# Kernel tuning notes

Hardware: AMD Instinct MI355X
Metric: run time of the kernel (lower is better)

Reference implementation:

```python
import jax, jax.numpy as jnp
import numpy as np

H = 64  # hidden_size
IN = 9  # input_size == output_size
PRED_LEN = 10
SRC_LEN = 7
B = 65536


def _lstm_step(x, h, c, Wih, Whh, b):
    # PyTorch gate order: i, f, g, o
    gates = x @ Wih.T + h @ Whh.T + b  # (B, 4H)
    i, f, g, o = jnp.split(gates, 4, axis=-1)
    i = jax.nn.sigmoid(i)
    f = jax.nn.sigmoid(f)
    g = jnp.tanh(g)
    o = jax.nn.sigmoid(o)
    c_new = f * c + i * g
    h_new = o * jnp.tanh(c_new)
    return h_new, c_new


def setup_inputs() -> dict:
    key = jax.random.key(0)
    ks = jax.random.split(key, 9)
    s = 1.0 / np.sqrt(H)  # torch LSTM init scale
    return {
        "src": jax.random.normal(ks[0], (B, SRC_LEN, IN), dtype=jnp.float32),
        "enc_Wih": jax.random.normal(ks[1], (4 * H, IN), dtype=jnp.float32) * s,
        "enc_Whh": jax.random.normal(ks[2], (4 * H, H), dtype=jnp.float32) * s,
        "enc_b": jax.random.normal(ks[3], (4 * H,), dtype=jnp.float32) * s,
        "dec_Wih": jax.random.normal(ks[4], (4 * H, IN), dtype=jnp.float32) * s,
        "dec_Whh": jax.random.normal(ks[5], (4 * H, H), dtype=jnp.float32) * s,
        "dec_b": jax.random.normal(ks[6], (4 * H,), dtype=jnp.float32) * s,
        "fc_W": jax.random.normal(ks[7], (IN, H), dtype=jnp.float32) * s,
        "fc_b": jax.random.normal(ks[8], (IN,), dtype=jnp.float32) * s,
    }


def reference(src, enc_Wih, enc_Whh, enc_b, dec_Wih, dec_Whh, dec_b, fc_W, fc_b):
    b = src.shape[0]
    h0 = jnp.zeros((b, H), dtype=src.dtype)
    c0 = jnp.zeros((b, H), dtype=src.dtype)

    # Encoder: scan over the 7 source timesteps
    def enc_f(carry, x_t):
        h, c = carry
        h, c = _lstm_step(x_t, h, c, enc_Wih, enc_Whh, enc_b)
        return (h, c), None

    (h, c), _ = jax.lax.scan(enc_f, (h0, c0), jnp.swapaxes(src, 0, 1))

    x_last = src[:, -1, :]  # (B, IN)

    def dec_f(carry, _):
        h, c, x = carry
        h, c = _lstm_step(x, h, c, dec_Wih, dec_Whh, dec_b)
        pred = h @ fc_W.T + fc_b  # (B, IN)
        return (h, c, pred), pred

    _, preds = jax.lax.scan(dec_f, (h, c, x_last), None, length=PRED_LEN)
    return jnp.swapaxes(preds, 0, 1)  # (B, PRED_LEN, IN)
```

## Files before the change

kernel.cpp:

```cpp
#include <hip/hip_runtime.h>
#include <hip/hip_bf16.h>
#include <stdint.h>

namespace {
constexpr int kH = 64;
constexpr int kIn = 9;
constexpr int kSrcLen = 7;
constexpr int kPredLen = 10;
constexpr int kRows = 64;
constexpr int kThreads = 256;
constexpr int kOutW = kPredLen * kIn;
constexpr int kABlk = 12;
constexpr int kASz = kABlk * kRows * 8;

typedef __attribute__((ext_vector_type(8))) _Float16 frag_a;
typedef __attribute__((ext_vector_type(4))) float frag_cd;

__device__ __forceinline__ float fast_rcp(float x) { return __builtin_amdgcn_rcpf(x); }
__device__ __forceinline__ float sigmoid_f(float x) { return fast_rcp(1.0f + __expf(-x)); }
__device__ __forceinline__ float tanh_f(float x) { return 1.0f - 2.0f * fast_rcp(__expf(2.0f * x) + 1.0f); }

__device__ __forceinline__ float ldf(const void* p, int i, int isbf) {
  if (isbf) {
    uint32_t w = ((uint32_t)((const uint16_t*)p)[i]) << 16;
    float f; __builtin_memcpy(&f, &w, 4); return f;
  }
  return ((const float*)p)[i];
}

__device__ __forceinline__ float gate_w(const void* Whh, const void* Wih,
                                        int n, int k, int isbf) {
  if (k < kH) return ldf(Whh, n * kH + k, isbf);
  if (k < kH + kIn) return ldf(Wih, n * kIn + (k - kH), isbf);
  return 0.0f;
}
}

extern "C" __global__ void detect_dtype_kernel(const uint16_t* __restrict__ src_u16,
                                               int* __restrict__ flag) {
  const int t = threadIdx.x;
  int bad = 0;
  for (int i = t; i < 256; i += 64) {
    const uint16_t u = src_u16[i];
    const uint32_t e = (u >> 7) & 0xFF;
    const int plausible = (u == 0) || (e >= 100 && e <= 150);
    bad += !plausible;
  }
#pragma unroll
  for (int off = 32; off; off >>= 1) bad += __shfl_down(bad, off, 64);
  if (t == 0) *flag = (bad < 64) ? 1 : 0;
}

extern "C" __global__ void __launch_bounds__(kThreads)
__attribute__((amdgpu_waves_per_eu(2, 2)))
lstm_seq2seq_kernel(const void* __restrict__ src,
                    const void* __restrict__ enc_Wih,
                    const void* __restrict__ enc_Whh,
                    const void* __restrict__ enc_b,
                    const void* __restrict__ dec_Wih,
                    const void* __restrict__ dec_Whh,
                    const void* __restrict__ dec_b,
                    const void* __restrict__ fc_W,
                    const void* __restrict__ fc_b,
                    void* __restrict__ out,
                    const int* __restrict__ flag) {
  __shared__ __align__(16) _Float16 a_m[2][kASz];

  const int tid = threadIdx.x;
  const int lane = tid & 63;
  const int wave = tid >> 6;
  const int quad = lane >> 4;
  const int half = lane & 15;
  const int row0 = blockIdx.x * kRows;
  const int isbf = *flag;
  const int col = wave * 16 + half;

  for (int i = tid; i < kASz; i += kThreads) {
    a_m[0][i] = (_Float16)0.0f;
    a_m[1][i] = (_Float16)0.0f;
  }
  __syncthreads();

  for (int item = tid; item < kRows * kIn; item += kThreads) {
    const int r = item / kIn, i = item - r * kIn;
    const float x = ldf(src, (row0 + r) * (kSrcLen * kIn) + i, isbf);
    a_m[0][(((8 + (i >> 3)) * kRows) + r) * 8 + (i & 7)] = (_Float16)x;
  }

  float c_st[16];
#pragma unroll
  for (int i = 0; i < 16; ++i) c_st[i] = 0.0f;

  frag_a bm[3][4];
  float bias_g[4];
  frag_a fm[2];
  float fcb = 0.0f;

  auto load_gate_frags = [&](const void* Whh, const void* Wih, const void* bv) {
#pragma unroll
    for (int kt = 0; kt < 3; ++kt) {
#pragma unroll
      for (int nt = 0; nt < 4; ++nt) {
        frag_a f;
        const int n = nt * kH + col;
#pragma unroll
        for (int j = 0; j < 8; ++j) {
          const int k = kt * 32 + quad * 8 + j;
          f[j] = (_Float16)gate_w(Whh, Wih, n, k, isbf);
        }
        bm[kt][nt] = f;
      }
    }
#pragma unroll
    for (int nt = 0; nt < 4; ++nt) bias_g[nt] = ldf(bv, nt * kH + col, isbf);
  };

  auto lstm_step = [&](int cur) {
#pragma unroll 1
    for (int ch = 0; ch < 4; ++ch) {
      const int r = ch * 16 + half;
      const frag_a a0 = *(const frag_a*)&a_m[cur][((0 * 4 + quad) * kRows + r) * 8];
      const frag_a a1 = *(const frag_a*)&a_m[cur][((1 * 4 + quad) * kRows + r) * 8];
      const frag_a a2 = *(const frag_a*)&a_m[cur][((2 * 4 + quad) * kRows + r) * 8];

      frag_cd acc[4];
#pragma unroll
      for (int nt = 0; nt < 4; ++nt) {
        const float b = bias_g[nt];
        frag_cd a = {b, b, b, b};
        a = __builtin_amdgcn_mfma_f32_16x16x32_f16(a0, bm[0][nt], a, 0, 0, 0);
        a = __builtin_amdgcn_mfma_f32_16x16x32_f16(a1, bm[1][nt], a, 0, 0, 0);
        a = __builtin_amdgcn_mfma_f32_16x16x32_f16(a2, bm[2][nt], a, 0, 0, 0);
        acc[nt] = a;
      }

#pragma unroll
      for (int j = 0; j < 4; ++j) {
        const float gi = acc[0][j];
        const float gf = acc[1][j];
        const float gg = acc[2][j];
        const float go = acc[3][j];
        float c = c_st[ch * 4 + j];
        c = fmaf(sigmoid_f(gf), c, sigmoid_f(gi) * tanh_f(gg));
        c_st[ch * 4 + j] = c;
        const float h = sigmoid_f(go) * tanh_f(c);
        const int rr = ch * 16 + quad * 4 + j;
        a_m[cur ^ 1][(((col >> 3) * kRows) + rr) * 8 + (col & 7)] = (_Float16)h;
      }
    }
  };

  load_gate_frags(enc_Whh, enc_Wih, enc_b);
  __syncthreads();

  int cur = 0;
#pragma unroll 1
  for (int s = 0; s < kSrcLen; ++s) {
    lstm_step(cur);
    const int ns = (s + 1 < kSrcLen) ? s + 1 : kSrcLen - 1;
    for (int item = tid; item < kRows * kIn; item += kThreads) {
      const int r = item / kIn, i = item - r * kIn;
      const float x = ldf(src, (row0 + r) * (kSrcLen * kIn) + ns * kIn + i, isbf);
      a_m[cur ^ 1][(((8 + (i >> 3)) * kRows) + r) * 8 + (i & 7)] = (_Float16)x;
    }
    __syncthreads();
    cur ^= 1;
  }

  load_gate_frags(dec_Whh, dec_Wih, dec_b);
#pragma unroll
  for (int kt = 0; kt < 2; ++kt) {
    frag_a f;
#pragma unroll
    for (int j = 0; j < 8; ++j) {
      const int k = kt * 32 + quad * 8 + j;
      const float v = (half < kIn) ? ldf(fc_W, half * kH + k, isbf) : 0.0f;
      f[j] = (_Float16)v;
    }
    fm[kt] = f;
  }
  fcb = (half < kIn) ? ldf(fc_b, half, isbf) : 0.0f;

#pragma unroll 1
  for (int t = 0; t < kPredLen; ++t) {
    lstm_step(cur);
    __syncthreads();
    cur ^= 1;

    const int r = wave * 16 + half;
    const frag_a a0 = *(const frag_a*)&a_m[cur][((0 * 4 + quad) * kRows + r) * 8];
    const frag_a a1 = *(const frag_a*)&a_m[cur][((1 * 4 + quad) * kRows + r) * 8];
    frag_cd p = {fcb, fcb, fcb, fcb};
    p = __builtin_amdgcn_mfma_f32_16x16x32_f16(a0, fm[0], p, 0, 0, 0);
    p = __builtin_amdgcn_mfma_f32_16x16x32_f16(a1, fm[1], p, 0, 0, 0);

    if (half < kIn) {
#pragma unroll
      for (int j = 0; j < 4; ++j) {
        const int rr = wave * 16 + quad * 4 + j;
        const float pred = p[j];
        const int oidx = (row0 + rr) * kOutW + t * kIn + half;
        if (isbf) {
          ((__hip_bfloat16*)out)[oidx] = __float2bfloat16(pred);
        } else {
          ((float*)out)[oidx] = pred;
        }
        a_m[cur][(((8 + (half >> 3)) * kRows) + rr) * 8 + (half & 7)] = (_Float16)pred;
      }
    }
    __syncthreads();
  }
}

extern "C" void kernel_launch(void* const* d_in, const int* in_sizes, int n_in,
                              void* d_out, int out_size, void* d_ws, size_t ws_size,
                              hipStream_t stream) {
  (void)n_in; (void)ws_size; (void)out_size;
  int* flag = (int*)d_ws;

  hipLaunchKernelGGL(detect_dtype_kernel, dim3(1), dim3(64), 0, stream,
                     (const uint16_t*)d_in[0], flag);

  const int b_total = in_sizes[0] / (kSrcLen * kIn);
  const int grid = b_total / kRows;

  hipLaunchKernelGGL(lstm_seq2seq_kernel, dim3(grid), dim3(kThreads), 0, stream,
                     d_in[0], d_in[1], d_in[2], d_in[3], d_in[4], d_in[5],
                     d_in[6], d_in[7], d_in[8], d_out, flag);
}
```

Baseline: 255.2 us.

## Fold bias into MFMA via constant-one column, prefetch src loads, raise occupancy

Puts the gate bias into the spare K slot 73 of the weight fragments and sets a constant 1.0 in the matching activation column, so the MFMA accumulators start at zero and no bias registers are needed. The next timestep's src values are now loaded into registers before the LSTM step runs, hiding global-load latency behind the MFMA work. The LDS and global index math is precomputed once per thread. The waves-per-EU hint goes from 2 to 3, which trades registers per thread for occupancy and risks spills given the large fragment arrays.

```diff
diff --git a/kernel.cpp b/kernel.cpp
--- a/kernel.cpp
+++ b/kernel.cpp
@@ -10,6 +10,7 @@
 constexpr int kRows = 64;
 constexpr int kThreads = 256;
 constexpr int kOutW = kPredLen * kIn;
+constexpr int kBiasK = 73;
 constexpr int kABlk = 12;
 constexpr int kASz = kABlk * kRows * 8;
 
@@ -29,9 +30,10 @@
 }
 
 __device__ __forceinline__ float gate_w(const void* Whh, const void* Wih,
-                                        int n, int k, int isbf) {
+                                        const void* bv, int n, int k, int isbf) {
   if (k < kH) return ldf(Whh, n * kH + k, isbf);
   if (k < kH + kIn) return ldf(Wih, n * kIn + (k - kH), isbf);
+  if (k == kBiasK) return ldf(bv, n, isbf);
   return 0.0f;
 }
 }
@@ -52,7 +54,7 @@
 }
 
 extern "C" __global__ void __launch_bounds__(kThreads)
-__attribute__((amdgpu_waves_per_eu(2, 2)))
+__attribute__((amdgpu_waves_per_eu(3, 3)))
 lstm_seq2seq_kernel(const void* __restrict__ src,
                     const void* __restrict__ enc_Wih,
                     const void* __restrict__ enc_Whh,
@@ -76,15 +78,30 @@
   const int col = wave * 16 + half;
 
   for (int i = tid; i < kASz; i += kThreads) {
-    a_m[0][i] = (_Float16)0.0f;
-    a_m[1][i] = (_Float16)0.0f;
+    const int e = i & 7;
+    const int blk = i / (kRows * 8);
+    const _Float16 v = (blk == 9 && e == 1) ? (_Float16)1.0f : (_Float16)0.0f;
+    a_m[0][i] = v;
+    a_m[1][i] = v;
   }
   __syncthreads();
 
-  for (int item = tid; item < kRows * kIn; item += kThreads) {
-    const int r = item / kIn, i = item - r * kIn;
-    const float x = ldf(src, (row0 + r) * (kSrcLen * kIn) + i, isbf);
-    a_m[0][(((8 + (i >> 3)) * kRows) + r) * 8 + (i & 7)] = (_Float16)x;
+  const int it1_on = (tid + 256 < kRows * kIn);
+  const int it2_on = (tid + 512 < kRows * kIn);
+  const int r_0 = tid / kIn, i_0 = tid - r_0 * kIn;
+  const int r_1 = (tid + 256) / kIn, i_1 = (tid + 256) - r_1 * kIn;
+  const int r_2 = (tid + 512) / kIn, i_2 = (tid + 512) - r_2 * kIn;
+  const int lds0 = (((8 + (i_0 >> 3)) * kRows) + r_0) * 8 + (i_0 & 7);
+  const int lds1 = (((8 + (i_1 >> 3)) * kRows) + r_1) * 8 + (i_1 & 7);
+  const int lds2 = (((8 + (i_2 >> 3)) * kRows) + r_2) * 8 + (i_2 & 7);
+  const int g0 = (row0 + r_0) * (kSrcLen * kIn) + i_0;
+  const int g1 = (row0 + r_1) * (kSrcLen * kIn) + i_1;
+  const int g2 = (row0 + r_2) * (kSrcLen * kIn) + i_2;
+
+  {
+    a_m[0][lds0] = (_Float16)ldf(src, g0, isbf);
+    if (it1_on) a_m[0][lds1] = (_Float16)ldf(src, g1, isbf);
+    if (it2_on) a_m[0][lds2] = (_Float16)ldf(src, g2, isbf);
   }
 
   float c_st[16];
@@ -92,7 +109,6 @@
   for (int i = 0; i < 16; ++i) c_st[i] = 0.0f;
 
   frag_a bm[3][4];
-  float bias_g[4];
   frag_a fm[2];
   float fcb = 0.0f;
 
@@ -106,13 +122,11 @@
 #pragma unroll
         for (int j = 0; j < 8; ++j) {
           const int k = kt * 32 + quad * 8 + j;
-          f[j] = (_Float16)gate_w(Whh, Wih, n, k, isbf);
+          f[j] = (_Float16)gate_w(Whh, Wih, bv, n, k, isbf);
         }
         bm[kt][nt] = f;
       }
     }
-#pragma unroll
-    for (int nt = 0; nt < 4; ++nt) bias_g[nt] = ldf(bv, nt * kH + col, isbf);
   };
 
   auto lstm_step = [&](int cur) {
@@ -126,8 +140,7 @@
       frag_cd acc[4];
 #pragma unroll
       for (int nt = 0; nt < 4; ++nt) {
-        const float b = bias_g[nt];
-        frag_cd a = {b, b, b, b};
+        frag_cd a = {0.f, 0.f, 0.f, 0.f};
         a = __builtin_amdgcn_mfma_f32_16x16x32_f16(a0, bm[0][nt], a, 0, 0, 0);
         a = __builtin_amdgcn_mfma_f32_16x16x32_f16(a1, bm[1][nt], a, 0, 0, 0);
         a = __builtin_amdgcn_mfma_f32_16x16x32_f16(a2, bm[2][nt], a, 0, 0, 0);
@@ -156,13 +169,17 @@
   int cur = 0;
 #pragma unroll 1
   for (int s = 0; s < kSrcLen; ++s) {
+    const int ns = (s + 1 < kSrcLen) ? s + 1 : kSrcLen - 1;
+    const int off = ns * kIn;
+    const float x0 = ldf(src, g0 + off, isbf);
+    const float x1 = it1_on ? ldf(src, g1 + off, isbf) : 0.0f;
+    const float x2 = it2_on ? ldf(src, g2 + off, isbf) : 0.0f;
+
     lstm_step(cur);
-    const int ns = (s + 1 < kSrcLen) ? s + 1 : kSrcLen - 1;
-    for (int item = tid; item < kRows * kIn; item += kThreads) {
-      const int r = item / kIn, i = item - r * kIn;
-      const float x = ldf(src, (row0 + r) * (kSrcLen * kIn) + ns * kIn + i, isbf);
-      a_m[cur ^ 1][(((8 + (i >> 3)) * kRows) + r) * 8 + (i & 7)] = (_Float16)x;
-    }
+
+    a_m[cur ^ 1][lds0] = (_Float16)x0;
+    if (it1_on) a_m[cur ^ 1][lds1] = (_Float16)x1;
+    if (it2_on) a_m[cur ^ 1][lds2] = (_Float16)x2;
     __syncthreads();
     cur ^= 1;
   }
```

New measurement: 250.2 us. -2.0%, faster.
